# Performance work log

Measured on AMD Instinct MI355X. Metric: run time of the kernel, lower is better.

The kernel has to match this reference:

```python
import jax, jax.numpy as jnp
import numpy as np

DIM, B, H, W = 96, 2, 64, 64
D_INNER, D_STATE, DT_RANK, K = 2 * DIM, 16, 6, 4


def _conv2d(x, w, b=None, padding=0, dilation=1, groups=1):
    out = jax.lax.conv_general_dilated(
        x, w, (1, 1), [(padding, padding)] * 2,
        rhs_dilation=(dilation, dilation),
        dimension_numbers=('NCHW', 'OIHW', 'NCHW'),
        feature_group_count=groups)
    return out if b is None else out + b[None, :, None, None]


def _layernorm(x, g, b, eps=1e-5):
    mu = x.mean(-1, keepdims=True)
    xc = x - mu
    var = (xc * xc).mean(-1, keepdims=True)
    return xc * jax.lax.rsqrt(var + eps) * g + b


def _chan_recal(t, w1, w2):
    s = t.mean((2, 3)) + t.max(axis=(2, 3))          # GAP + GMP, (B,C)
    w = jax.nn.sigmoid(jax.nn.relu(s @ w1.T) @ w2.T)
    return t * w[:, :, None, None]


def _selective_scan(u, delta, A, Bm, Cm, D):
    # u, delta: (B,K,d,L); A: (K,d,N); Bm,Cm: (B,K,N,L); D: (K,d)
    Bsz, Kk, d, L = u.shape
    N = A.shape[-1]
    seq = (jnp.moveaxis(delta, -1, 0), jnp.moveaxis(u, -1, 0),
           jnp.moveaxis(Bm, -1, 0), jnp.moveaxis(Cm, -1, 0))
    h0 = jnp.zeros((Bsz, Kk, d, N), u.dtype)

    def step(h, inp):
        dl, ul, bl, cl = inp  # (B,K,d),(B,K,d),(B,K,N),(B,K,N)
        h = jnp.exp(dl[..., None] * A) * h + (dl * ul)[..., None] * bl[:, :, None, :]
        return h, (h * cl[:, :, None, :]).sum(-1)

    _, ys = jax.lax.scan(step, h0, seq)
    return jnp.moveaxis(ys, 0, -1) + D[None, :, :, None] * u  # (B,K,d,L)


def _ss2d(x, in_proj_w, conv_w, conv_b, x_proj_w, dt_w, dt_b,
          A_logs, Ds, out_norm_g, out_norm_b, out_proj_w):
    Bsz, Hh, Ww, C = x.shape
    d = in_proj_w.shape[0] // 2
    xm, z = jnp.split(x @ in_proj_w.T, 2, axis=-1)
    xm = jnp.transpose(xm, (0, 3, 1, 2))  # (B,d,H,W)
    xm = jax.nn.silu(_conv2d(xm, conv_w, conv_b, padding=1, groups=d))
    L = Hh * Ww
    x_hw = xm.reshape(Bsz, d, L)
    x_wh = jnp.transpose(xm, (0, 1, 3, 2)).reshape(Bsz, d, L)
    xs = jnp.stack([x_hw, x_wh, x_hw[..., ::-1], x_wh[..., ::-1]], axis=1)  # (B,4,d,L)
    x_dbl = jnp.einsum('bkdl,kcd->bkcl', xs, x_proj_w)
    r = dt_w.shape[-1]
    N = A_logs.shape[-1]
    dts, Bs, Cs = jnp.split(x_dbl, [r, r + N], axis=2)
    dts = jax.nn.softplus(jnp.einsum('bkrl,kdr->bkdl', dts, dt_w) + dt_b[None, :, :, None])
    out_y = _selective_scan(xs, dts, -jnp.exp(A_logs), Bs, Cs, Ds)
    inv_y = out_y[:, 2:4, :, ::-1]
    wh = lambda t: jnp.transpose(t.reshape(Bsz, d, Ww, Hh), (0, 1, 3, 2)).reshape(Bsz, d, L)
    y = out_y[:, 0] + inv_y[:, 0] + wh(out_y[:, 1]) + wh(inv_y[:, 1])
    y = _layernorm(jnp.transpose(y, (0, 2, 1)).reshape(Bsz, Hh, Ww, d), out_norm_g, out_norm_b)
    return (y * jax.nn.silu(z)) @ out_proj_w.T


def _forward(x, arf_w1, arf_b1, arf_w2, arf_b2, arf_w3, arf_b3, arf_w4, arf_b4,
             fuse_w, fuse_b, edge_w, enh_w1, enh_b1, bn_g, bn_b, enh_w2, enh_b2,
             pre_fc1, pre_fc2, norm_g, norm_b, in_proj_w, ss_conv_w, ss_conv_b,
             x_proj_w, dt_w, dt_b, A_logs, Ds, out_norm_g, out_norm_b, out_proj_w,
             post_fc1, post_fc2, proj_w, proj_b):
    shortcut = x
    C = x.shape[1]
    g = C // 4
    # AdaptiveReceptiveField (fc gating branch is dead code in the original forward)
    f1 = _conv2d(x, arf_w1, arf_b1, padding=1, dilation=1, groups=g)
    f2 = _conv2d(x, arf_w2, arf_b2, padding=2, dilation=2, groups=g)
    f3 = _conv2d(x, arf_w3, arf_b3, padding=4, dilation=4, groups=g)
    f4 = _conv2d(x, arf_w4, arf_b4, padding=8, dilation=8, groups=g)
    h = _conv2d(jnp.concatenate([f1, f2, f3, f4], 1), fuse_w, fuse_b)
    # LearnableEdgeEnhancement (BatchNorm in training mode: batch stats, biased var)
    edge = _conv2d(h, edge_w, None, padding=1, groups=C)
    e = _conv2d(edge, enh_w1, enh_b1)
    mu = e.mean((0, 2, 3), keepdims=True)
    var = ((e - mu) ** 2).mean((0, 2, 3), keepdims=True)
    e = jax.nn.relu((e - mu) * jax.lax.rsqrt(var + 1e-5) * bn_g[None, :, None, None]
                    + bn_b[None, :, None, None])
    h = h * (1.0 + jax.nn.sigmoid(_conv2d(e, enh_w2, enh_b2)))
    h = _chan_recal(h, pre_fc1, pre_fc2)
    hn = _layernorm(jnp.transpose(h, (0, 2, 3, 1)), norm_g, norm_b)
    hn = _ss2d(hn, in_proj_w, ss_conv_w, ss_conv_b, x_proj_w, dt_w, dt_b,
               A_logs, Ds, out_norm_g, out_norm_b, out_proj_w)
    h = jnp.transpose(hn, (0, 3, 1, 2))
    h = _chan_recal(h, post_fc1, post_fc2)
    h = _conv2d(h, proj_w, proj_b)
    return shortcut + h


def setup_inputs():
    key = jax.random.key(0)
    ks = iter(jax.random.split(key, 48))
    rn = lambda shape, s=0.05: jax.random.normal(next(ks), shape, jnp.float32) * s
    lap = jnp.array([[0., 1., 0.], [1., -4., 1.], [0., 1., 0.]], jnp.float32)
    q = DIM // 4
    inp = {
        'x': jax.random.normal(next(ks), (B, DIM, H, W), jnp.float32),
        'arf_w1': rn((q, 4, 3, 3)), 'arf_b1': rn((q,)),
        'arf_w2': rn((q, 4, 3, 3)), 'arf_b2': rn((q,)),
        'arf_w3': rn((q, 4, 3, 3)), 'arf_b3': rn((q,)),
        'arf_w4': rn((q, 4, 3, 3)), 'arf_b4': rn((q,)),
        'fuse_w': rn((DIM, DIM, 1, 1)), 'fuse_b': rn((DIM,)),
        'edge_w': jnp.tile(lap[None, None], (DIM, 1, 1, 1)),
        'enh_w1': rn((q, DIM, 1, 1)), 'enh_b1': rn((q,)),
        'bn_g': jnp.ones((q,), jnp.float32), 'bn_b': jnp.zeros((q,), jnp.float32),
        'enh_w2': rn((DIM, q, 1, 1)), 'enh_b2': rn((DIM,)),
        'pre_fc1': rn((q, DIM)), 'pre_fc2': rn((DIM, q)),
        'norm_g': jnp.ones((DIM,), jnp.float32), 'norm_b': jnp.zeros((DIM,), jnp.float32),
        'in_proj_w': rn((2 * D_INNER, DIM)),
        'ss_conv_w': rn((D_INNER, 1, 3, 3)), 'ss_conv_b': rn((D_INNER,)),
        'x_proj_w': rn((K, DT_RANK + 2 * D_STATE, D_INNER)),
        'dt_w': rn((K, D_INNER, DT_RANK), 0.1), 'dt_b': rn((K, D_INNER), 0.1),
        'A_logs': jnp.broadcast_to(jnp.log(jnp.arange(1, D_STATE + 1, dtype=jnp.float32)),
                                   (K, D_INNER, D_STATE)) + jnp.zeros((K, D_INNER, D_STATE), jnp.float32),
        'Ds': jnp.ones((K, D_INNER), jnp.float32),
        'out_norm_g': jnp.ones((D_INNER,), jnp.float32),
        'out_norm_b': jnp.zeros((D_INNER,), jnp.float32),
        'out_proj_w': rn((DIM, D_INNER)),
        'post_fc1': rn((q, DIM)), 'post_fc2': rn((DIM, q)),
        'proj_w': rn((DIM, DIM, 1, 1)), 'proj_b': rn((DIM,)),
    }
    return inp


def reference(x, arf_w1, arf_b1, arf_w2, arf_b2, arf_w3, arf_b3, arf_w4, arf_b4,
              fuse_w, fuse_b, edge_w, enh_w1, enh_b1, bn_g, bn_b, enh_w2, enh_b2,
              pre_fc1, pre_fc2, norm_g, norm_b, in_proj_w, ss_conv_w, ss_conv_b,
              x_proj_w, dt_w, dt_b, A_logs, Ds, out_norm_g, out_norm_b, out_proj_w,
              post_fc1, post_fc2, proj_w, proj_b):
    return _forward(x, arf_w1, arf_b1, arf_w2, arf_b2, arf_w3, arf_b3, arf_w4, arf_b4,
                    fuse_w, fuse_b, edge_w, enh_w1, enh_b1, bn_g, bn_b, enh_w2, enh_b2,
                    pre_fc1, pre_fc2, norm_g, norm_b, in_proj_w, ss_conv_w, ss_conv_b,
                    x_proj_w, dt_w, dt_b, A_logs, Ds, out_norm_g, out_norm_b, out_proj_w,
                    post_fc1, post_fc2, proj_w, proj_b)
```

## Files before the change

kernel.cpp:

```cpp
#include <hip/hip_runtime.h>
#include <cmath>

#define LL   4096
#define HWD  64
#define CCH  96
#define QQ   24
#define DDI  192
#define NST  16
#define NCH  128
#define CLEN 32
#define TSC  32
#define XT2  32
#define XP   108
#define FP   100

static const size_t OFF_F   = 0;
static const size_t OFF_H   = 786432;
static const size_t OFF_E   = 1572864;
static const size_t OFF_BN  = 1769472;
static const size_t OFF_S1  = 1769536;
static const size_t OFF_W1  = 1769728;
static const size_t OFF_S2  = 1769920;
static const size_t OFF_W2  = 1770112;
static const size_t OFF_HN  = 1770304;
static const size_t OFF_XM  = 2556736;
static const size_t OFF_Z   = 4129600;
static const size_t OFF_XC  = 5702464;
static const size_t OFF_DTS = 7275328;
static const size_t OFF_BC  = 13566784;
static const size_t OFF_YK  = 14615360;
static const size_t OFF_Y2  = 22528832;
static const size_t OFF_HL  = 23315264;
static const size_t OFF_SD  = 26460992;
static const size_t OFF_HIN = 26657600;

static __device__ __forceinline__ int map_k(int k, int l) {
  int ll = (k & 2) ? (LL - 1 - l) : l;
  return (k & 1) ? (((ll & 63) << 6) | (ll >> 6)) : ll;
}

__global__ __launch_bounds__(256) void k_arf(const float* __restrict__ x,
    const float* __restrict__ w1, const float* __restrict__ b1,
    const float* __restrict__ w2, const float* __restrict__ b2,
    const float* __restrict__ w3, const float* __restrict__ b3,
    const float* __restrict__ w4, const float* __restrict__ b4,
    float* __restrict__ f) {
  int idx = blockIdx.x * 256 + threadIdx.x;
  int p = idx & (LL - 1);
  int oc = __builtin_amdgcn_readfirstlane((idx >> 12) % CCH);
  int b  = __builtin_amdgcn_readfirstlane(idx / (CCH * LL));
  int i = oc / QQ, q = oc % QQ;
  int dil = 1 << i;
  const float* w  = (i == 0 ? w1 : i == 1 ? w2 : i == 2 ? w3 : w4) + q * 36;
  const float* bb = (i == 0 ? b1 : i == 1 ? b2 : i == 2 ? b3 : b4);
  int yy0 = p >> 6, xx0 = p & 63;
  float acc = bb[q];
  const float* xin = x + ((size_t)b * CCH + q * 4) * LL;
  #pragma unroll
  for (int ky = 0; ky < 3; ky++) {
    int yy = yy0 + (ky - 1) * dil;
    if (yy < 0 || yy >= HWD) continue;
    #pragma unroll
    for (int kx = 0; kx < 3; kx++) {
      int xx = xx0 + (kx - 1) * dil;
      if (xx < 0 || xx >= HWD) continue;
      int pp = (yy << 6) + xx;
      #pragma unroll
      for (int ci = 0; ci < 4; ci++)
        acc += w[ci * 9 + ky * 3 + kx] * xin[(size_t)ci * LL + pp];
    }
  }
  f[idx] = acc;
}

__global__ __launch_bounds__(256) void k_fuse(const float* __restrict__ f,
    const float* __restrict__ fw, const float* __restrict__ fb, float* __restrict__ h) {
  int pix0 = blockIdx.x * 64;
  int oc0 = blockIdx.y * 48;
  int b = pix0 >> 12, p0 = pix0 & (LL - 1);
  int t = threadIdx.x;
  __shared__ float fs[64][FP];
  __shared__ float wbuf[48 * 96];
  for (int i = t; i < 96 * 16; i += 256) {
    int c = i >> 4, q = i & 15;
    float4 v = *(const float4*)(f + ((size_t)b * CCH + c) * LL + p0 + q * 4);
    fs[q * 4 + 0][c] = v.x; fs[q * 4 + 1][c] = v.y;
    fs[q * 4 + 2][c] = v.z; fs[q * 4 + 3][c] = v.w;
  }
  {
    const float4* src = (const float4*)(fw + (size_t)oc0 * CCH);
    float4* dst = (float4*)wbuf;
    for (int i = t; i < 48 * 24; i += 256) dst[i] = src[i];
  }
  __syncthreads();
  int px = t & 63;
  int cg = __builtin_amdgcn_readfirstlane(t >> 6);
  float acc[12];
  #pragma unroll
  for (int j = 0; j < 12; j++) acc[j] = 0.f;
  for (int c4 = 0; c4 < 24; c4++) {
    float4 xv = *(const float4*)(&fs[px][c4 * 4]);
    #pragma unroll
    for (int j = 0; j < 12; j++) {
      float4 wv = *(const float4*)(&wbuf[(cg * 12 + j) * 96 + c4 * 4]);
      acc[j] = fmaf(xv.x, wv.x, fmaf(xv.y, wv.y, fmaf(xv.z, wv.z, fmaf(xv.w, wv.w, acc[j]))));
    }
  }
  __syncthreads();
  float* ot = &fs[0][0];
  #pragma unroll
  for (int j = 0; j < 12; j++) ot[px * 49 + cg * 12 + j] = acc[j];
  __syncthreads();
  for (int i = t; i < 48 * 64; i += 256) {
    int o = i >> 6, p2 = i & 63;
    h[((size_t)b * CCH + oc0 + o) * LL + p0 + p2] = ot[p2 * 49 + o] + fb[oc0 + o];
  }
}

__global__ __launch_bounds__(256) void k_edge(const float* __restrict__ h,
    const float* __restrict__ ew, float* __restrict__ edge) {
  int idx = blockIdx.x * 256 + threadIdx.x;
  int p = idx & (LL - 1);
  int c = __builtin_amdgcn_readfirstlane((idx >> 12) % CCH);
  int b = __builtin_amdgcn_readfirstlane(idx / (CCH * LL));
  int yy0 = p >> 6, xx0 = p & 63;
  const float* w = ew + c * 9;
  const float* hr = h + ((size_t)b * CCH + c) * LL;
  float acc = 0.f;
  #pragma unroll
  for (int ky = 0; ky < 3; ky++) {
    int yy = yy0 + ky - 1;
    if (yy < 0 || yy >= HWD) continue;
    #pragma unroll
    for (int kx = 0; kx < 3; kx++) {
      int xx = xx0 + kx - 1;
      if (xx < 0 || xx >= HWD) continue;
      acc += w[ky * 3 + kx] * hr[(yy << 6) + xx];
    }
  }
  edge[idx] = acc;
}

__global__ __launch_bounds__(256) void k_e1(const float* __restrict__ edge,
    const float* __restrict__ w, const float* __restrict__ bias, float* __restrict__ e) {
  int idx = blockIdx.x * 256 + threadIdx.x;
  int p = idx & (LL - 1);
  int q = __builtin_amdgcn_readfirstlane((idx >> 12) % QQ);
  int b = __builtin_amdgcn_readfirstlane(idx / (QQ * LL));
  const float* er = edge + (size_t)b * CCH * LL + p;
  const float* wr = w + q * CCH;
  float acc = bias[q];
  for (int c = 0; c < CCH; c++) acc += wr[c] * er[(size_t)c * LL];
  e[idx] = acc;
}

__global__ __launch_bounds__(256) void k_bnstats(const float* __restrict__ e,
    const float* __restrict__ g, const float* __restrict__ bb, float* __restrict__ bn) {
  int q = blockIdx.x, tid = threadIdx.x;
  __shared__ float rs[256], r2[256];
  float s = 0.f, s2 = 0.f;
  for (int b = 0; b < 2; b++) {
    const float* er = e + ((size_t)b * QQ + q) * LL;
    for (int p = tid; p < LL; p += 256) { float v = er[p]; s += v; s2 += v * v; }
  }
  rs[tid] = s; r2[tid] = s2; __syncthreads();
  for (int st = 128; st > 0; st >>= 1) {
    if (tid < st) { rs[tid] += rs[tid + st]; r2[tid] += r2[tid + st]; }
    __syncthreads();
  }
  if (tid == 0) {
    float mu = rs[0] / (2.f * LL);
    float var = r2[0] / (2.f * LL) - mu * mu;
    float sc = g[q] * rsqrtf(var + 1e-5f);
    bn[q] = sc;
    bn[QQ + q] = bb[q] - mu * sc;
  }
}

__global__ __launch_bounds__(256) void k_enh(const float* __restrict__ e,
    const float* __restrict__ bn, const float* __restrict__ w2,
    const float* __restrict__ b2, float* __restrict__ h) {
  int idx = blockIdx.x * 256 + threadIdx.x;
  int p = idx & (LL - 1);
  int o = __builtin_amdgcn_readfirstlane((idx >> 12) % CCH);
  int b = __builtin_amdgcn_readfirstlane(idx / (CCH * LL));
  const float* er = e + (size_t)b * QQ * LL + p;
  const float* wr = w2 + o * QQ;
  float acc = b2[o];
  #pragma unroll
  for (int q = 0; q < QQ; q++) {
    float en = fmaxf(er[(size_t)q * LL] * bn[q] + bn[QQ + q], 0.f);
    acc += wr[q] * en;
  }
  float sig = 1.f / (1.f + __expf(-acc));
  h[idx] *= (1.f + sig);
}

__global__ __launch_bounds__(256) void k_rowreduce(const float* __restrict__ t, float* __restrict__ sout) {
  int row = blockIdx.x, tid = threadIdx.x;
  __shared__ float rs[256], rm[256];
  float s = 0.f, m = -3.402823466e38f;
  const float* tr = t + (size_t)row * LL;
  for (int p = tid; p < LL; p += 256) { float v = tr[p]; s += v; m = fmaxf(m, v); }
  rs[tid] = s; rm[tid] = m; __syncthreads();
  for (int st = 128; st > 0; st >>= 1) {
    if (tid < st) { rs[tid] += rs[tid + st]; rm[tid] = fmaxf(rm[tid], rm[tid + st]); }
    __syncthreads();
  }
  if (tid == 0) sout[row] = rs[0] / (float)LL + rm[0];
}

__global__ __launch_bounds__(128) void k_recal_fc(const float* __restrict__ s1,
    const float* __restrict__ fc1, const float* __restrict__ fc2, float* __restrict__ wout) {
  int b = blockIdx.x, tid = threadIdx.x;
  __shared__ float sv[CCH];
  __shared__ float hid[QQ];
  if (tid < CCH) sv[tid] = s1[b * CCH + tid];
  __syncthreads();
  if (tid < QQ) {
    float a = 0.f;
    for (int c = 0; c < CCH; c++) a += sv[c] * fc1[tid * CCH + c];
    hid[tid] = fmaxf(a, 0.f);
  }
  __syncthreads();
  if (tid < CCH) {
    float a = 0.f;
    #pragma unroll
    for (int q = 0; q < QQ; q++) a += hid[q] * fc2[tid * QQ + q];
    wout[b * CCH + tid] = 1.f / (1.f + __expf(-a));
  }
}

__global__ __launch_bounds__(256) void k_recal_ln(const float* __restrict__ h,
    const float* __restrict__ w1buf, const float* __restrict__ ng,
    const float* __restrict__ nb, float* __restrict__ hn) {
  int pix = blockIdx.x * 4 + (threadIdx.x >> 6);
  int b = pix >> 12, p = pix & (LL - 1);
  int l = threadIdx.x & 63;
  float v0 = h[((size_t)b * CCH + l) * LL + p] * w1buf[b * CCH + l];
  float v1 = 0.f;
  if (l < 32) v1 = h[((size_t)b * CCH + 64 + l) * LL + p] * w1buf[b * CCH + 64 + l];
  float s = v0 + v1;
  #pragma unroll
  for (int o = 32; o > 0; o >>= 1) s += __shfl_xor(s, o);
  float mu = s / (float)CCH;
  float q = (v0 - mu) * (v0 - mu);
  if (l < 32) q += (v1 - mu) * (v1 - mu);
  #pragma unroll
  for (int o = 32; o > 0; o >>= 1) q += __shfl_xor(q, o);
  float rs = rsqrtf(q / (float)CCH + 1e-5f);
  float* dst = hn + ((size_t)b * LL + p) * CCH;
  dst[l] = (v0 - mu) * rs * ng[l] + nb[l];
  if (l < 32) dst[64 + l] = (v1 - mu) * rs * ng[64 + l] + nb[64 + l];
}

__global__ __launch_bounds__(256) void k_inproj(const float* __restrict__ hn,
    const float* __restrict__ W, float* __restrict__ xm, float* __restrict__ z) {
  int pix0 = blockIdx.x * 64;
  int oc0 = blockIdx.y * CCH;
  int t = threadIdx.x;
  __shared__ float xs[64][XP];
  __shared__ float wbuf[CCH * CCH];
  for (int i = t; i < 64 * 24; i += 256) {
    int row = i / 24, dq = i % 24;
    *(float4*)(&xs[row][dq * 4]) = *(const float4*)(hn + (size_t)(pix0 + row) * CCH + dq * 4);
  }
  {
    const float4* src = (const float4*)(W + (size_t)oc0 * CCH);
    float4* dst = (float4*)wbuf;
    for (int i = t; i < CCH * 24; i += 256) dst[i] = src[i];
  }
  __syncthreads();
  int li = t & 63;
  int cg = __builtin_amdgcn_readfirstlane(t >> 6);
  float acc[24];
  #pragma unroll
  for (int j = 0; j < 24; j++) acc[j] = 0.f;
  for (int dq = 0; dq < 24; dq++) {
    float4 xv = *(const float4*)(&xs[li][dq * 4]);
    #pragma unroll
    for (int j = 0; j < 24; j++) {
      float4 wv = *(const float4*)(&wbuf[(cg + 4 * j) * CCH + dq * 4]);
      acc[j] = fmaf(xv.x, wv.x, fmaf(xv.y, wv.y, fmaf(xv.z, wv.z, fmaf(xv.w, wv.w, acc[j]))));
    }
  }
  __syncthreads();
  float* ot = &xs[0][0];
  #pragma unroll
  for (int j = 0; j < 24; j++) ot[li * 97 + cg + 4 * j] = acc[j];
  __syncthreads();
  float* dst = (oc0 < DDI) ? xm : z;
  int od0 = oc0 % DDI;
  for (int i = t; i < 64 * 96; i += 256) {
    int row = i / 96, c = i % 96;
    dst[(size_t)(pix0 + row) * DDI + od0 + c] = ot[row * 97 + c];
  }
}

__global__ __launch_bounds__(256) void k_ssconv(const float* __restrict__ xm,
    const float* __restrict__ w, const float* __restrict__ bias, float* __restrict__ xc) {
  int idx = blockIdx.x * 256 + threadIdx.x;
  int d = idx % DDI;
  int rem = idx / DDI;
  int xx0 = rem & 63;
  int y0 = ((rem >> 6) & 31) * 2;
  int b = idx / (DDI * LL / 2);
  float wv[9];
  #pragma unroll
  for (int i = 0; i < 9; i++) wv[i] = w[d * 9 + i];
  float acc0 = bias[d], acc1 = bias[d];
  const float* xr = xm + (size_t)b * LL * DDI + d;
  #pragma unroll
  for (int ky = -1; ky <= 2; ky++) {
    int yy = y0 + ky;
    if (yy < 0 || yy >= HWD) continue;
    #pragma unroll
    for (int kx = -1; kx <= 1; kx++) {
      int xx = xx0 + kx;
      if (xx < 0 || xx >= HWD) continue;
      float val = xr[(size_t)((yy << 6) + xx) * DDI];
      if (ky <= 1) acc0 += wv[(ky + 1) * 3 + (kx + 1)] * val;
      if (ky >= 0) acc1 += wv[ky * 3 + (kx + 1)] * val;
    }
  }
  size_t o0 = ((size_t)b * LL + (y0 << 6) + xx0) * DDI + d;
  xc[o0] = acc0 / (1.f + __expf(-acc0));
  xc[o0 + 64 * DDI] = acc1 / (1.f + __expf(-acc1));
}

__global__ __launch_bounds__(256) void k_xdbl(const float* __restrict__ xc,
    const float* __restrict__ xpw, float* __restrict__ dtr_ws, float* __restrict__ bcb) {
  int lt = blockIdx.x;
  int bk = blockIdx.y;
  int b = bk >> 2, k = bk & 3;
  int t = threadIdx.x;
  __shared__ float xs[XT2][XP];
  __shared__ float wbuf[38 * 96];
  int l0 = lt * XT2;
  int pos = t & 31;
  int cg = t >> 5;
  float acc[5];
  #pragma unroll
  for (int j = 0; j < 5; j++) acc[j] = 0.f;
  for (int h = 0; h < 2; h++) {
    __syncthreads();
    for (int i = t; i < XT2 * 24; i += 256) {
      int row = i / 24, dq = i % 24;
      int p = map_k(k, l0 + row);
      *(float4*)(&xs[row][dq * 4]) =
          *(const float4*)(xc + ((size_t)b * LL + p) * DDI + h * 96 + dq * 4);
    }
    for (int i = t; i < 38 * 24; i += 256) {
      int c = i / 24, dq = i % 24;
      *(float4*)(&wbuf[c * 96 + dq * 4]) =
          *(const float4*)(xpw + ((size_t)k * 38 + c) * DDI + h * 96 + dq * 4);
    }
    __syncthreads();
    for (int dq = 0; dq < 24; dq++) {
      float4 xv = *(const float4*)(&xs[pos][dq * 4]);
      #pragma unroll
      for (int j = 0; j < 5; j++) {
        int c = cg + 8 * j;
        if (c < 38) {
          float4 wv = *(const float4*)(&wbuf[c * 96 + dq * 4]);
          acc[j] = fmaf(xv.x, wv.x, fmaf(xv.y, wv.y, fmaf(xv.z, wv.z, fmaf(xv.w, wv.w, acc[j]))));
        }
      }
    }
  }
  #pragma unroll
  for (int j = 0; j < 5; j++) {
    int c = cg + 8 * j;
    if (c < 6) dtr_ws[((size_t)bk * LL + l0 + pos) * 6 + c] = acc[j];
    else if (c < 38) bcb[((size_t)bk * LL + l0 + pos) * 32 + (c - 6)] = acc[j];
  }
}

template <int PASS>
__global__ __launch_bounds__(192) void k_scan(const float* __restrict__ dtr_ws,
    const float* __restrict__ bcb, const float* __restrict__ xc,
    const float* __restrict__ A_logs, const float* __restrict__ dtw,
    const float* __restrict__ dtb, float* __restrict__ hl, float* __restrict__ sd,
    const float* __restrict__ hin, float* __restrict__ yk) {
  int ch = blockIdx.x, bk = blockIdx.y;
  int b = bk >> 2, k = bk & 3;
  int d = threadIdx.x;
  __shared__ float u_s[TSC][DDI];
  __shared__ float bcs[TSC][32];
  __shared__ float dtr_s[TSC][6];
  float Av[NST];
  #pragma unroll
  for (int n = 0; n < NST; n++) Av[n] = -__expf(A_logs[(size_t)(k * DDI + d) * NST + n]);
  bool pw = true;
  #pragma unroll
  for (int n = 1; n < NST; n++) pw = pw && (fabsf(Av[n] - (float)(n + 1) * Av[0]) <= 1e-3f * (n + 1));
  float wdt[6];
  #pragma unroll
  for (int r = 0; r < 6; r++) wdt[r] = dtw[((size_t)(k * DDI + d)) * 6 + r];
  float bdt = dtb[k * DDI + d];
  float h[NST];
  if (PASS == 0) {
    #pragma unroll
    for (int n = 0; n < NST; n++) h[n] = 0.f;
  } else {
    const float* hp = hin + ((size_t)(bk * DDI + d) * NCH + ch) * NST;
    #pragma unroll
    for (int n = 0; n < NST; n++) h[n] = hp[n];
  }
  float sumdt = 0.f;
  int l0 = ch * CLEN;
  {
    for (int i = d; i < TSC * (DDI / 4); i += 192) {
      int row = i / (DDI / 4), q = i % (DDI / 4);
      int p = map_k(k, l0 + row);
      ((float4*)u_s)[i] = *(const float4*)(xc + ((size_t)b * LL + p) * DDI + q * 4);
    }
    {
      const float4* src = (const float4*)(bcb + ((size_t)bk * LL + l0) * 32);
      float4* dst = (float4*)bcs;
      for (int i = d; i < TSC * 32 / 4; i += 192) dst[i] = src[i];
    }
    for (int i = d; i < TSC * 6; i += 192)
      ((float*)dtr_s)[i] = dtr_ws[((size_t)bk * LL + l0) * 6 + i];
    __syncthreads();
    for (int tt = 0; tt < TSC; tt++) {
      float a = bdt;
      #pragma unroll
      for (int r = 0; r < 6; r++) a = fmaf(wdt[r], dtr_s[tt][r], a);
      float dt = (a > 15.f) ? a : __logf(1.f + __expf(a));
      float u  = u_s[tt][d];
      float dtu = dt * u;
      if (PASS == 0) sumdt += dt;
      float eA[NST];
      if (pw) {
        float E = __expf(dt * Av[0]);
        float en = 1.f;
        #pragma unroll
        for (int n = 0; n < NST; n++) { en *= E; eA[n] = en; }
      } else {
        #pragma unroll
        for (int n = 0; n < NST; n++) eA[n] = __expf(dt * Av[n]);
      }
      float y = 0.f;
      #pragma unroll
      for (int n = 0; n < NST; n++) {
        h[n] = eA[n] * h[n] + dtu * bcs[tt][n];
        y += h[n] * bcs[tt][16 + n];
      }
      if (PASS == 1) {
        int p = map_k(k, l0 + tt);
        yk[((size_t)bk * LL + p) * DDI + d] = y;
      }
    }
  }
  if (PASS == 0) {
    float* hp = hl + ((size_t)(bk * DDI + d) * NCH + ch) * NST;
    #pragma unroll
    for (int n = 0; n < NST; n++) hp[n] = h[n];
    sd[(size_t)(bk * DDI + d) * NCH + ch] = sumdt;
  }
}

__global__ __launch_bounds__(256) void k_carry(const float* __restrict__ A_logs,
    const float* __restrict__ hl, const float* __restrict__ sd, float* __restrict__ hin) {
  int idx = blockIdx.x * 256 + threadIdx.x;
  int n = idx & 15;
  int d = (idx >> 4) % DDI;
  int bk = idx / (DDI * NST);
  int k = bk & 3;
  float Aval = -__expf(A_logs[(size_t)(k * DDI + d) * NST + n]);
  float h = 0.f;
  size_t base = (size_t)(bk * DDI + d) * NCH;
  for (int ch = 0; ch < NCH; ch++) {
    hin[(base + ch) * NST + n] = h;
    h = __expf(Aval * sd[base + ch]) * h + hl[(base + ch) * NST + n];
  }
}

__global__ __launch_bounds__(256) void k_combine(const float* __restrict__ yk,
    const float* __restrict__ xc, const float* __restrict__ Ds, const float* __restrict__ z,
    const float* __restrict__ ong, const float* __restrict__ onb, float* __restrict__ g) {
  int pix = blockIdx.x * 4 + (threadIdx.x >> 6);
  int b = pix >> 12, p = pix & (LL - 1);
  int l = threadIdx.x & 63;
  float v[3];
  #pragma unroll
  for (int m = 0; m < 3; m++) {
    int d = l + 64 * m;
    size_t base = ((size_t)b * 4 * LL + p) * DDI + d;
    float tv = yk[base] + yk[base + (size_t)LL * DDI] + yk[base + 2ul * LL * DDI] + yk[base + 3ul * LL * DDI];
    tv += (Ds[d] + Ds[DDI + d] + Ds[2 * DDI + d] + Ds[3 * DDI + d]) * xc[((size_t)b * LL + p) * DDI + d];
    v[m] = tv;
  }
  float s = v[0] + v[1] + v[2];
  #pragma unroll
  for (int o = 32; o > 0; o >>= 1) s += __shfl_xor(s, o);
  float mu = s / (float)DDI;
  float q = 0.f;
  #pragma unroll
  for (int m = 0; m < 3; m++) q += (v[m] - mu) * (v[m] - mu);
  #pragma unroll
  for (int o = 32; o > 0; o >>= 1) q += __shfl_xor(q, o);
  float rs = rsqrtf(q / (float)DDI + 1e-5f);
  #pragma unroll
  for (int m = 0; m < 3; m++) {
    int d = l + 64 * m;
    float yv = (v[m] - mu) * rs * ong[d] + onb[d];
    float zz = z[((size_t)b * LL + p) * DDI + d];
    g[((size_t)b * LL + p) * DDI + d] = yv * (zz / (1.f + __expf(-zz)));
  }
}

__global__ __launch_bounds__(256) void k_outproj(const float* __restrict__ g,
    const float* __restrict__ W, float* __restrict__ y2) {
  int pix0 = blockIdx.x * 64;
  int oc0 = blockIdx.y * 48;
  int b = pix0 >> 12, p0 = pix0 & (LL - 1);
  int t = threadIdx.x;
  __shared__ float xs[64][XP];
  __shared__ float wbuf[48 * 96];
  int li = t & 63;
  int cg = __builtin_amdgcn_readfirstlane(t >> 6);
  float acc[12];
  #pragma unroll
  for (int j = 0; j < 12; j++) acc[j] = 0.f;
  for (int h = 0; h < 2; h++) {
    __syncthreads();
    for (int i = t; i < 64 * 24; i += 256) {
      int row = i / 24, dq = i % 24;
      *(float4*)(&xs[row][dq * 4]) =
          *(const float4*)(g + (size_t)(pix0 + row) * DDI + h * 96 + dq * 4);
    }
    for (int i = t; i < 48 * 24; i += 256) {
      int c = i / 24, dq = i % 24;
      *(float4*)(&wbuf[c * 96 + dq * 4]) =
          *(const float4*)(W + (size_t)(oc0 + c) * DDI + h * 96 + dq * 4);
    }
    __syncthreads();
    for (int dq = 0; dq < 24; dq++) {
      float4 xv = *(const float4*)(&xs[li][dq * 4]);
      #pragma unroll
      for (int j = 0; j < 12; j++) {
        float4 wv = *(const float4*)(&wbuf[(cg + 4 * j) * 96 + dq * 4]);
        acc[j] = fmaf(xv.x, wv.x, fmaf(xv.y, wv.y, fmaf(xv.z, wv.z, fmaf(xv.w, wv.w, acc[j]))));
      }
    }
  }
  __syncthreads();
  float* ot = &xs[0][0];
  #pragma unroll
  for (int j = 0; j < 12; j++) ot[li * 49 + cg + 4 * j] = acc[j];
  __syncthreads();
  for (int i = t; i < 48 * 64; i += 256) {
    int o = i / 64, pi = i % 64;
    y2[((size_t)b * CCH + oc0 + o) * LL + p0 + pi] = ot[pi * 49 + o];
  }
}

__global__ __launch_bounds__(256) void k_final(const float* __restrict__ x,
    const float* __restrict__ y2, const float* __restrict__ w2buf,
    const float* __restrict__ pw, const float* __restrict__ pb, float* __restrict__ out) {
  int pix0 = blockIdx.x * 64;
  int oc0 = blockIdx.y * 48;
  int b = pix0 >> 12, p0 = pix0 & (LL - 1);
  int t = threadIdx.x;
  __shared__ float fs[64][FP];
  __shared__ float wbuf[48 * 96];
  for (int i = t; i < 96 * 16; i += 256) {
    int c = i >> 4, q = i & 15;
    float4 v = *(const float4*)(y2 + ((size_t)b * CCH + c) * LL + p0 + q * 4);
    fs[q * 4 + 0][c] = v.x; fs[q * 4 + 1][c] = v.y;
    fs[q * 4 + 2][c] = v.z; fs[q * 4 + 3][c] = v.w;
  }
  for (int i = t; i < 48 * 24; i += 256) {
    int row = i / 24, q = i % 24;
    float4 wv = *(const float4*)(pw + (size_t)(oc0 + row) * CCH + q * 4);
    float4 cv = *(const float4*)(w2buf + b * CCH + q * 4);
    ((float4*)wbuf)[i] = make_float4(wv.x * cv.x, wv.y * cv.y, wv.z * cv.z, wv.w * cv.w);
  }
  __syncthreads();
  int px = t & 63;
  int cg = __builtin_amdgcn_readfirstlane(t >> 6);
  float acc[12];
  #pragma unroll
  for (int j = 0; j < 12; j++) acc[j] = 0.f;
  for (int c4 = 0; c4 < 24; c4++) {
    float4 xv = *(const float4*)(&fs[px][c4 * 4]);
    #pragma unroll
    for (int j = 0; j < 12; j++) {
      float4 wv = *(const float4*)(&wbuf[(cg * 12 + j) * 96 + c4 * 4]);
      acc[j] = fmaf(xv.x, wv.x, fmaf(xv.y, wv.y, fmaf(xv.z, wv.z, fmaf(xv.w, wv.w, acc[j]))));
    }
  }
  __syncthreads();
  float* ot = &fs[0][0];
  #pragma unroll
  for (int j = 0; j < 12; j++) ot[px * 49 + cg * 12 + j] = acc[j];
  __syncthreads();
  for (int i = t; i < 48 * 64; i += 256) {
    int o = i >> 6, p2 = i & 63;
    size_t oi = ((size_t)b * CCH + oc0 + o) * LL + p0 + p2;
    out[oi] = x[oi] + pb[oc0 + o] + ot[p2 * 49 + o];
  }
}

extern "C" void kernel_launch(void* const* d_in, const int* in_sizes, int n_in,
                              void* d_out, int out_size, void* d_ws, size_t ws_size,
                              hipStream_t stream) {
  const float* x        = (const float*)d_in[0];
  const float* arf_w1   = (const float*)d_in[1];
  const float* arf_b1   = (const float*)d_in[2];
  const float* arf_w2   = (const float*)d_in[3];
  const float* arf_b2   = (const float*)d_in[4];
  const float* arf_w3   = (const float*)d_in[5];
  const float* arf_b3   = (const float*)d_in[6];
  const float* arf_w4   = (const float*)d_in[7];
  const float* arf_b4   = (const float*)d_in[8];
  const float* fuse_w   = (const float*)d_in[9];
  const float* fuse_b   = (const float*)d_in[10];
  const float* edge_w   = (const float*)d_in[11];
  const float* enh_w1   = (const float*)d_in[12];
  const float* enh_b1   = (const float*)d_in[13];
  const float* bn_g     = (const float*)d_in[14];
  const float* bn_b     = (const float*)d_in[15];
  const float* enh_w2   = (const float*)d_in[16];
  const float* enh_b2   = (const float*)d_in[17];
  const float* pre_fc1  = (const float*)d_in[18];
  const float* pre_fc2  = (const float*)d_in[19];
  const float* norm_g   = (const float*)d_in[20];
  const float* norm_b   = (const float*)d_in[21];
  const float* in_proj_w= (const float*)d_in[22];
  const float* ss_conv_w= (const float*)d_in[23];
  const float* ss_conv_b= (const float*)d_in[24];
  const float* x_proj_w = (const float*)d_in[25];
  const float* dt_w     = (const float*)d_in[26];
  const float* dt_b     = (const float*)d_in[27];
  const float* A_logs   = (const float*)d_in[28];
  const float* Ds       = (const float*)d_in[29];
  const float* out_ng   = (const float*)d_in[30];
  const float* out_nb   = (const float*)d_in[31];
  const float* out_proj_w = (const float*)d_in[32];
  const float* post_fc1 = (const float*)d_in[33];
  const float* post_fc2 = (const float*)d_in[34];
  const float* proj_w   = (const float*)d_in[35];
  const float* proj_b   = (const float*)d_in[36];

  float* ws = (float*)d_ws;
  float* fbuf  = ws + OFF_F;
  float* hbuf  = ws + OFF_H;
  float* ebuf  = ws + OFF_E;
  float* bnbuf = ws + OFF_BN;
  float* s1buf = ws + OFF_S1;
  float* w1buf = ws + OFF_W1;
  float* s2buf = ws + OFF_S2;
  float* w2buf = ws + OFF_W2;
  float* hnbuf = ws + OFF_HN;
  float* xmbuf = ws + OFF_XM;
  float* zbuf  = ws + OFF_Z;
  float* xcbuf = ws + OFF_XC;
  float* dtrbuf= ws + OFF_DTS;
  float* bcbuf = ws + OFF_BC;
  float* ykbuf = ws + OFF_YK;
  float* hlbuf = ws + OFF_HL;
  float* sdbuf = ws + OFF_SD;
  float* hinbuf= ws + OFF_HIN;
  float* y2buf = ws + OFF_Y2;
  float* gbuf  = xmbuf;

  k_arf<<<3072, 256, 0, stream>>>(x, arf_w1, arf_b1, arf_w2, arf_b2, arf_w3, arf_b3, arf_w4, arf_b4, fbuf);
  k_fuse<<<dim3(128, 2), 256, 0, stream>>>(fbuf, fuse_w, fuse_b, hbuf);
  k_edge<<<3072, 256, 0, stream>>>(hbuf, edge_w, fbuf);
  k_e1<<<768, 256, 0, stream>>>(fbuf, enh_w1, enh_b1, ebuf);
  k_bnstats<<<24, 256, 0, stream>>>(ebuf, bn_g, bn_b, bnbuf);
  k_enh<<<3072, 256, 0, stream>>>(ebuf, bnbuf, enh_w2, enh_b2, hbuf);
  k_rowreduce<<<192, 256, 0, stream>>>(hbuf, s1buf);
  k_recal_fc<<<2, 128, 0, stream>>>(s1buf, pre_fc1, pre_fc2, w1buf);
  k_recal_ln<<<2048, 256, 0, stream>>>(hbuf, w1buf, norm_g, norm_b, hnbuf);
  k_inproj<<<dim3(128, 4), 256, 0, stream>>>(hnbuf, in_proj_w, xmbuf, zbuf);
  k_ssconv<<<3072, 256, 0, stream>>>(xmbuf, ss_conv_w, ss_conv_b, xcbuf);
  k_xdbl<<<dim3(LL / XT2, 8), 256, 0, stream>>>(xcbuf, x_proj_w, dtrbuf, bcbuf);
  k_scan<0><<<dim3(NCH, 8), 192, 0, stream>>>(dtrbuf, bcbuf, xcbuf, A_logs, dt_w, dt_b, hlbuf, sdbuf, nullptr, nullptr);
  k_carry<<<96, 256, 0, stream>>>(A_logs, hlbuf, sdbuf, hinbuf);
  k_scan<1><<<dim3(NCH, 8), 192, 0, stream>>>(dtrbuf, bcbuf, xcbuf, A_logs, dt_w, dt_b, nullptr, nullptr, hinbuf, ykbuf);
  k_combine<<<2048, 256, 0, stream>>>(ykbuf, xcbuf, Ds, zbuf, out_ng, out_nb, gbuf);
  k_outproj<<<dim3(128, 2), 256, 0, stream>>>(gbuf, out_proj_w, y2buf);
  k_rowreduce<<<192, 256, 0, stream>>>(y2buf, s2buf);
  k_recal_fc<<<2, 128, 0, stream>>>(s2buf, post_fc1, post_fc2, w2buf);
  k_final<<<dim3(128, 2), 256, 0, stream>>>(x, y2buf, w2buf, proj_w, proj_b, (float*)d_out);
  (void)in_sizes; (void)n_in; (void)out_size; (void)ws_size;
}
```

Baseline: 241.7 us.

## Fuse channel-recalibration reductions, FC and layernorms into neighbouring GEMM kernels

Global sum/max reductions now come from per-block partials written by k_enh and k_outproj. The recalibration FC layers are recomputed inside each consuming block of k_inproj and k_final. The pre-norm layernorm moves into k_inproj, and the combine plus out_norm plus SiLU gating moves into k_outproj. This removes six launches and the intermediate hn and g round trips through global memory. In exchange, every block redundantly runs the small FC layers, the variance is computed in a single pass, and the shared-memory footprint grows.

```diff
diff --git a/kernel.cpp b/kernel.cpp
--- a/kernel.cpp
+++ b/kernel.cpp
@@ -13,16 +13,12 @@
 #define XT2  32
 #define XP   108
 #define FP   100
+#define VP   204
 
 static const size_t OFF_F   = 0;
 static const size_t OFF_H   = 786432;
 static const size_t OFF_E   = 1572864;
 static const size_t OFF_BN  = 1769472;
-static const size_t OFF_S1  = 1769536;
-static const size_t OFF_W1  = 1769728;
-static const size_t OFF_S2  = 1769920;
-static const size_t OFF_W2  = 1770112;
-static const size_t OFF_HN  = 1770304;
 static const size_t OFF_XM  = 2556736;
 static const size_t OFF_Z   = 4129600;
 static const size_t OFF_XC  = 5702464;
@@ -33,6 +29,10 @@
 static const size_t OFF_HL  = 23315264;
 static const size_t OFF_SD  = 26460992;
 static const size_t OFF_HIN = 26657600;
+static const size_t OFF_S1PS= 29803328;
+static const size_t OFF_S1PM= 29806400;
+static const size_t OFF_S2PS= 29809472;
+static const size_t OFF_S2PM= 29821760;
 
 static __device__ __forceinline__ int map_k(int k, int l) {
   int ll = (k & 2) ? (LL - 1 - l) : l;
@@ -179,8 +179,10 @@
 
 __global__ __launch_bounds__(256) void k_enh(const float* __restrict__ e,
     const float* __restrict__ bn, const float* __restrict__ w2,
-    const float* __restrict__ b2, float* __restrict__ h) {
-  int idx = blockIdx.x * 256 + threadIdx.x;
+    const float* __restrict__ b2, float* __restrict__ h,
+    float* __restrict__ s1ps, float* __restrict__ s1pm) {
+  int tid = threadIdx.x;
+  int idx = blockIdx.x * 256 + tid;
   int p = idx & (LL - 1);
   int o = __builtin_amdgcn_readfirstlane((idx >> 12) % CCH);
   int b = __builtin_amdgcn_readfirstlane(idx / (CCH * LL));
@@ -193,82 +195,96 @@
     acc += wr[q] * en;
   }
   float sig = 1.f / (1.f + __expf(-acc));
-  h[idx] *= (1.f + sig);
-}
-
-__global__ __launch_bounds__(256) void k_rowreduce(const float* __restrict__ t, float* __restrict__ sout) {
-  int row = blockIdx.x, tid = threadIdx.x;
-  __shared__ float rs[256], rm[256];
-  float s = 0.f, m = -3.402823466e38f;
-  const float* tr = t + (size_t)row * LL;
-  for (int p = tid; p < LL; p += 256) { float v = tr[p]; s += v; m = fmaxf(m, v); }
-  rs[tid] = s; rm[tid] = m; __syncthreads();
+  float val = h[idx] * (1.f + sig);
+  h[idx] = val;
+  __shared__ float rsum[256], rmax[256];
+  rsum[tid] = val; rmax[tid] = val; __syncthreads();
   for (int st = 128; st > 0; st >>= 1) {
-    if (tid < st) { rs[tid] += rs[tid + st]; rm[tid] = fmaxf(rm[tid], rm[tid + st]); }
+    if (tid < st) { rsum[tid] += rsum[tid + st]; rmax[tid] = fmaxf(rmax[tid], rmax[tid + st]); }
     __syncthreads();
   }
-  if (tid == 0) sout[row] = rs[0] / (float)LL + rm[0];
-}
-
-__global__ __launch_bounds__(128) void k_recal_fc(const float* __restrict__ s1,
-    const float* __restrict__ fc1, const float* __restrict__ fc2, float* __restrict__ wout) {
-  int b = blockIdx.x, tid = threadIdx.x;
-  __shared__ float sv[CCH];
-  __shared__ float hid[QQ];
-  if (tid < CCH) sv[tid] = s1[b * CCH + tid];
-  __syncthreads();
-  if (tid < QQ) {
-    float a = 0.f;
-    for (int c = 0; c < CCH; c++) a += sv[c] * fc1[tid * CCH + c];
-    hid[tid] = fmaxf(a, 0.f);
-  }
-  __syncthreads();
-  if (tid < CCH) {
-    float a = 0.f;
-    #pragma unroll
-    for (int q = 0; q < QQ; q++) a += hid[q] * fc2[tid * QQ + q];
-    wout[b * CCH + tid] = 1.f / (1.f + __expf(-a));
-  }
-}
-
-__global__ __launch_bounds__(256) void k_recal_ln(const float* __restrict__ h,
-    const float* __restrict__ w1buf, const float* __restrict__ ng,
-    const float* __restrict__ nb, float* __restrict__ hn) {
-  int pix = blockIdx.x * 4 + (threadIdx.x >> 6);
-  int b = pix >> 12, p = pix & (LL - 1);
-  int l = threadIdx.x & 63;
-  float v0 = h[((size_t)b * CCH + l) * LL + p] * w1buf[b * CCH + l];
-  float v1 = 0.f;
-  if (l < 32) v1 = h[((size_t)b * CCH + 64 + l) * LL + p] * w1buf[b * CCH + 64 + l];
-  float s = v0 + v1;
-  #pragma unroll
-  for (int o = 32; o > 0; o >>= 1) s += __shfl_xor(s, o);
-  float mu = s / (float)CCH;
-  float q = (v0 - mu) * (v0 - mu);
-  if (l < 32) q += (v1 - mu) * (v1 - mu);
-  #pragma unroll
-  for (int o = 32; o > 0; o >>= 1) q += __shfl_xor(q, o);
-  float rs = rsqrtf(q / (float)CCH + 1e-5f);
-  float* dst = hn + ((size_t)b * LL + p) * CCH;
-  dst[l] = (v0 - mu) * rs * ng[l] + nb[l];
-  if (l < 32) dst[64 + l] = (v1 - mu) * rs * ng[64 + l] + nb[64 + l];
-}
-
-__global__ __launch_bounds__(256) void k_inproj(const float* __restrict__ hn,
+  if (tid == 0) {
+    int row = blockIdx.x >> 4, blk = blockIdx.x & 15;
+    s1ps[row * 16 + blk] = rsum[0];
+    s1pm[row * 16 + blk] = rmax[0];
+  }
+}
+
+__global__ __launch_bounds__(256) void k_inproj(const float* __restrict__ h,
+    const float* __restrict__ s1ps, const float* __restrict__ s1pm,
+    const float* __restrict__ fc1, const float* __restrict__ fc2,
+    const float* __restrict__ ng, const float* __restrict__ nb,
     const float* __restrict__ W, float* __restrict__ xm, float* __restrict__ z) {
   int pix0 = blockIdx.x * 64;
   int oc0 = blockIdx.y * CCH;
+  int b = pix0 >> 12, p0 = pix0 & (LL - 1);
   int t = threadIdx.x;
   __shared__ float xs[64][XP];
   __shared__ float wbuf[CCH * CCH];
-  for (int i = t; i < 64 * 24; i += 256) {
-    int row = i / 24, dq = i % 24;
-    *(float4*)(&xs[row][dq * 4]) = *(const float4*)(hn + (size_t)(pix0 + row) * CCH + dq * 4);
-  }
+  __shared__ float wsm[CCH];
+  __shared__ float hid[QQ];
+  __shared__ float ps[64][4], ps2[64][4];
+  __shared__ float mu_s[64], rs_s[64];
+  if (t < CCH) {
+    const float4* sp = (const float4*)(s1ps + (size_t)(b * CCH + t) * 16);
+    const float4* mp = (const float4*)(s1pm + (size_t)(b * CCH + t) * 16);
+    float s = 0.f, m = -3.402823466e38f;
+    #pragma unroll
+    for (int i = 0; i < 4; i++) {
+      float4 a = sp[i]; s += a.x + a.y + a.z + a.w;
+      float4 c = mp[i]; m = fmaxf(m, fmaxf(fmaxf(c.x, c.y), fmaxf(c.z, c.w)));
+    }
+    wsm[t] = s / (float)LL + m;
+  }
+  __syncthreads();
+  if (t < QQ) {
+    float a = 0.f;
+    for (int c = 0; c < CCH; c++) a += wsm[c] * fc1[t * CCH + c];
+    hid[t] = fmaxf(a, 0.f);
+  }
+  __syncthreads();
+  float w1v = 0.f;
+  if (t < CCH) {
+    float a = 0.f;
+    #pragma unroll
+    for (int q = 0; q < QQ; q++) a += hid[q] * fc2[t * QQ + q];
+    w1v = 1.f / (1.f + __expf(-a));
+  }
+  __syncthreads();
+  if (t < CCH) wsm[t] = w1v;
   {
     const float4* src = (const float4*)(W + (size_t)oc0 * CCH);
     float4* dst = (float4*)wbuf;
     for (int i = t; i < CCH * 24; i += 256) dst[i] = src[i];
+  }
+  __syncthreads();
+  for (int i = t; i < CCH * 16; i += 256) {
+    int c = i >> 4, q = i & 15;
+    float w = wsm[c];
+    float4 v = *(const float4*)(h + ((size_t)b * CCH + c) * LL + p0 + q * 4);
+    xs[q * 4 + 0][c] = v.x * w; xs[q * 4 + 1][c] = v.y * w;
+    xs[q * 4 + 2][c] = v.z * w; xs[q * 4 + 3][c] = v.w * w;
+  }
+  __syncthreads();
+  {
+    int px = t & 63, qr = t >> 6;
+    float s = 0.f, s2 = 0.f;
+    #pragma unroll
+    for (int j = 0; j < 24; j++) { float v = xs[px][qr * 24 + j]; s += v; s2 += v * v; }
+    ps[px][qr] = s; ps2[px][qr] = s2;
+  }
+  __syncthreads();
+  if (t < 64) {
+    float ss = ps[t][0] + ps[t][1] + ps[t][2] + ps[t][3];
+    float ss2 = ps2[t][0] + ps2[t][1] + ps2[t][2] + ps2[t][3];
+    float mu = ss / (float)CCH;
+    mu_s[t] = mu;
+    rs_s[t] = rsqrtf(ss2 / (float)CCH - mu * mu + 1e-5f);
+  }
+  __syncthreads();
+  for (int i = t; i < 64 * CCH; i += 256) {
+    int px = i / CCH, c = i % CCH;
+    xs[px][c] = (xs[px][c] - mu_s[px]) * rs_s[px] * ng[c] + nb[c];
   }
   __syncthreads();
   int li = t & 63;
@@ -477,68 +493,96 @@
   }
 }
 
-__global__ __launch_bounds__(256) void k_combine(const float* __restrict__ yk,
+__global__ __launch_bounds__(256) void k_outproj(const float* __restrict__ yk,
     const float* __restrict__ xc, const float* __restrict__ Ds, const float* __restrict__ z,
-    const float* __restrict__ ong, const float* __restrict__ onb, float* __restrict__ g) {
-  int pix = blockIdx.x * 4 + (threadIdx.x >> 6);
-  int b = pix >> 12, p = pix & (LL - 1);
-  int l = threadIdx.x & 63;
-  float v[3];
-  #pragma unroll
-  for (int m = 0; m < 3; m++) {
-    int d = l + 64 * m;
-    size_t base = ((size_t)b * 4 * LL + p) * DDI + d;
-    float tv = yk[base] + yk[base + (size_t)LL * DDI] + yk[base + 2ul * LL * DDI] + yk[base + 3ul * LL * DDI];
-    tv += (Ds[d] + Ds[DDI + d] + Ds[2 * DDI + d] + Ds[3 * DDI + d]) * xc[((size_t)b * LL + p) * DDI + d];
-    v[m] = tv;
-  }
-  float s = v[0] + v[1] + v[2];
-  #pragma unroll
-  for (int o = 32; o > 0; o >>= 1) s += __shfl_xor(s, o);
-  float mu = s / (float)DDI;
-  float q = 0.f;
-  #pragma unroll
-  for (int m = 0; m < 3; m++) q += (v[m] - mu) * (v[m] - mu);
-  #pragma unroll
-  for (int o = 32; o > 0; o >>= 1) q += __shfl_xor(q, o);
-  float rs = rsqrtf(q / (float)DDI + 1e-5f);
-  #pragma unroll
-  for (int m = 0; m < 3; m++) {
-    int d = l + 64 * m;
-    float yv = (v[m] - mu) * rs * ong[d] + onb[d];
-    float zz = z[((size_t)b * LL + p) * DDI + d];
-    g[((size_t)b * LL + p) * DDI + d] = yv * (zz / (1.f + __expf(-zz)));
-  }
-}
-
-__global__ __launch_bounds__(256) void k_outproj(const float* __restrict__ g,
-    const float* __restrict__ W, float* __restrict__ y2) {
+    const float* __restrict__ ong, const float* __restrict__ onb,
+    const float* __restrict__ W, float* __restrict__ y2,
+    float* __restrict__ s2ps, float* __restrict__ s2pm) {
   int pix0 = blockIdx.x * 64;
   int oc0 = blockIdx.y * 48;
   int b = pix0 >> 12, p0 = pix0 & (LL - 1);
   int t = threadIdx.x;
-  __shared__ float xs[64][XP];
+  __shared__ float xs[64][VP];
   __shared__ float wbuf[48 * 96];
-  int li = t & 63;
-  int cg = __builtin_amdgcn_readfirstlane(t >> 6);
+  __shared__ float dsum[DDI];
+  __shared__ float ps[64][4], ps2[64][4];
+  __shared__ float mu_s[64], rs_s[64];
+  if (t < 48) {
+    float4 a  = *(const float4*)(Ds + t * 4);
+    float4 c1 = *(const float4*)(Ds + DDI + t * 4);
+    float4 c2 = *(const float4*)(Ds + 2 * DDI + t * 4);
+    float4 c3 = *(const float4*)(Ds + 3 * DDI + t * 4);
+    *(float4*)(&dsum[t * 4]) = make_float4(a.x + c1.x + c2.x + c3.x, a.y + c1.y + c2.y + c3.y,
+                                           a.z + c1.z + c2.z + c3.z, a.w + c1.w + c2.w + c3.w);
+  }
+  __syncthreads();
+  int px = t & 63, qr = t >> 6;
+  int p = p0 + px;
+  size_t pb = ((size_t)b * LL + p) * DDI;
+  size_t yb = ((size_t)b * 4 * LL + p) * DDI;
+  {
+    float s = 0.f, s2 = 0.f;
+    #pragma unroll
+    for (int j = 0; j < 12; j++) {
+      int c = (qr * 12 + j) * 4;
+      float4 y0 = *(const float4*)(yk + yb + c);
+      float4 y1 = *(const float4*)(yk + yb + (size_t)LL * DDI + c);
+      float4 y2v = *(const float4*)(yk + yb + 2ul * LL * DDI + c);
+      float4 y3 = *(const float4*)(yk + yb + 3ul * LL * DDI + c);
+      float4 u = *(const float4*)(xc + pb + c);
+      float4 dv = *(const float4*)(&dsum[c]);
+      float4 v;
+      v.x = y0.x + y1.x + y2v.x + y3.x + dv.x * u.x;
+      v.y = y0.y + y1.y + y2v.y + y3.y + dv.y * u.y;
+      v.z = y0.z + y1.z + y2v.z + y3.z + dv.z * u.z;
+      v.w = y0.w + y1.w + y2v.w + y3.w + dv.w * u.w;
+      *(float4*)(&xs[px][c]) = v;
+      s += v.x + v.y + v.z + v.w;
+      s2 += v.x * v.x + v.y * v.y + v.z * v.z + v.w * v.w;
+    }
+    ps[px][qr] = s; ps2[px][qr] = s2;
+  }
+  __syncthreads();
+  if (t < 64) {
+    float ss = ps[t][0] + ps[t][1] + ps[t][2] + ps[t][3];
+    float ss2 = ps2[t][0] + ps2[t][1] + ps2[t][2] + ps2[t][3];
+    float mu = ss / (float)DDI;
+    mu_s[t] = mu;
+    rs_s[t] = rsqrtf(ss2 / (float)DDI - mu * mu + 1e-5f);
+  }
+  __syncthreads();
+  {
+    float mu = mu_s[px], rs = rs_s[px];
+    #pragma unroll
+    for (int j = 0; j < 12; j++) {
+      int c = (qr * 12 + j) * 4;
+      float4 v = *(const float4*)(&xs[px][c]);
+      float4 zz = *(const float4*)(z + pb + c);
+      float4 og = *(const float4*)(ong + c);
+      float4 ob = *(const float4*)(onb + c);
+      float4 gv;
+      gv.x = ((v.x - mu) * rs * og.x + ob.x) * (zz.x / (1.f + __expf(-zz.x)));
+      gv.y = ((v.y - mu) * rs * og.y + ob.y) * (zz.y / (1.f + __expf(-zz.y)));
+      gv.z = ((v.z - mu) * rs * og.z + ob.z) * (zz.z / (1.f + __expf(-zz.z)));
+      gv.w = ((v.w - mu) * rs * og.w + ob.w) * (zz.w / (1.f + __expf(-zz.w)));
+      *(float4*)(&xs[px][c]) = gv;
+    }
+  }
+  int li = px;
+  int cg = __builtin_amdgcn_readfirstlane(qr);
   float acc[12];
   #pragma unroll
   for (int j = 0; j < 12; j++) acc[j] = 0.f;
-  for (int h = 0; h < 2; h++) {
+  for (int hh = 0; hh < 2; hh++) {
     __syncthreads();
-    for (int i = t; i < 64 * 24; i += 256) {
-      int row = i / 24, dq = i % 24;
-      *(float4*)(&xs[row][dq * 4]) =
-          *(const float4*)(g + (size_t)(pix0 + row) * DDI + h * 96 + dq * 4);
-    }
     for (int i = t; i < 48 * 24; i += 256) {
       int c = i / 24, dq = i % 24;
       *(float4*)(&wbuf[c * 96 + dq * 4]) =
-          *(const float4*)(W + (size_t)(oc0 + c) * DDI + h * 96 + dq * 4);
+          *(const float4*)(W + (size_t)(oc0 + c) * DDI + hh * 96 + dq * 4);
     }
     __syncthreads();
     for (int dq = 0; dq < 24; dq++) {
-      float4 xv = *(const float4*)(&xs[li][dq * 4]);
+      float4 xv = *(const float4*)(&xs[li][hh * 96 + dq * 4]);
       #pragma unroll
       for (int j = 0; j < 12; j++) {
         float4 wv = *(const float4*)(&wbuf[(cg + 4 * j) * 96 + dq * 4]);
@@ -546,6 +590,22 @@
       }
     }
   }
+  int lane = t & 63;
+  #pragma unroll
+  for (int j = 0; j < 12; j++) {
+    float sv = acc[j], mv = acc[j];
+    #pragma unroll
+    for (int o = 32; o > 0; o >>= 1) {
+      sv += __shfl_xor(sv, o);
+      mv = fmaxf(mv, __shfl_xor(mv, o));
+    }
+    if (lane == 0) {
+      int oc = oc0 + cg + 4 * j;
+      int tile = blockIdx.x & 63;
+      s2ps[(size_t)(b * CCH + oc) * 64 + tile] = sv;
+      s2pm[(size_t)(b * CCH + oc) * 64 + tile] = mv;
+    }
+  }
   __syncthreads();
   float* ot = &xs[0][0];
   #pragma unroll
@@ -558,7 +618,8 @@
 }
 
 __global__ __launch_bounds__(256) void k_final(const float* __restrict__ x,
-    const float* __restrict__ y2, const float* __restrict__ w2buf,
+    const float* __restrict__ y2, const float* __restrict__ s2ps, const float* __restrict__ s2pm,
+    const float* __restrict__ fc1, const float* __restrict__ fc2,
     const float* __restrict__ pw, const float* __restrict__ pb, float* __restrict__ out) {
   int pix0 = blockIdx.x * 64;
   int oc0 = blockIdx.y * 48;
@@ -566,6 +627,36 @@
   int t = threadIdx.x;
   __shared__ float fs[64][FP];
   __shared__ float wbuf[48 * 96];
+  __shared__ float wsm[CCH];
+  __shared__ float hid[QQ];
+  if (t < CCH) {
+    const float4* sp = (const float4*)(s2ps + (size_t)(b * CCH + t) * 64);
+    const float4* mp = (const float4*)(s2pm + (size_t)(b * CCH + t) * 64);
+    float s = 0.f, m = -3.402823466e38f;
+    #pragma unroll
+    for (int i = 0; i < 16; i++) {
+      float4 a = sp[i]; s += a.x + a.y + a.z + a.w;
+      float4 c = mp[i]; m = fmaxf(m, fmaxf(fmaxf(c.x, c.y), fmaxf(c.z, c.w)));
+    }
+    wsm[t] = s / (float)LL + m;
+  }
+  __syncthreads();
+  if (t < QQ) {
+    float a = 0.f;
+    for (int c = 0; c < CCH; c++) a += wsm[c] * fc1[t * CCH + c];
+    hid[t] = fmaxf(a, 0.f);
+  }
+  __syncthreads();
+  float w2v = 0.f;
+  if (t < CCH) {
+    float a = 0.f;
+    #pragma unroll
+    for (int q = 0; q < QQ; q++) a += hid[q] * fc2[t * QQ + q];
+    w2v = 1.f / (1.f + __expf(-a));
+  }
+  __syncthreads();
+  if (t < CCH) wsm[t] = w2v;
+  __syncthreads();
   for (int i = t; i < 96 * 16; i += 256) {
     int c = i >> 4, q = i & 15;
     float4 v = *(const float4*)(y2 + ((size_t)b * CCH + c) * LL + p0 + q * 4);
@@ -575,8 +666,8 @@
   for (int i = t; i < 48 * 24; i += 256) {
     int row = i / 24, q = i % 24;
     float4 wv = *(const float4*)(pw + (size_t)(oc0 + row) * CCH + q * 4);
-    float4 cv = *(const float4*)(w2buf + b * CCH + q * 4);
-    ((float4*)wbuf)[i] = make_float4(wv.x * cv.x, wv.y * cv.y, wv.z * cv.z, wv.w * cv.w);
+    ((float4*)wbuf)[i] = make_float4(wv.x * wsm[q * 4], wv.y * wsm[q * 4 + 1],
+                                     wv.z * wsm[q * 4 + 2], wv.w * wsm[q * 4 + 3]);
   }
   __syncthreads();
   int px = t & 63;
@@ -650,42 +741,34 @@
   float* hbuf  = ws + OFF_H;
   float* ebuf  = ws + OFF_E;
   float* bnbuf = ws + OFF_BN;
-  float* s1buf = ws + OFF_S1;
-  float* w1buf = ws + OFF_W1;
-  float* s2buf = ws + OFF_S2;
-  float* w2buf = ws + OFF_W2;
-  float* hnbuf = ws + OFF_HN;
   float* xmbuf = ws + OFF_XM;
   float* zbuf  = ws + OFF_Z;
   float* xcbuf = ws + OFF_XC;
   float* dtrbuf= ws + OFF_DTS;
   float* bcbuf = ws + OFF_BC;
   float* ykbuf = ws + OFF_YK;
+  float* y2buf = ws + OFF_Y2;
   float* hlbuf = ws + OFF_HL;
   float* sdbuf = ws + OFF_SD;
   float* hinbuf= ws + OFF_HIN;
-  float* y2buf = ws + OFF_Y2;
-  float* gbuf  = xmbuf;
+  float* s1ps  = ws + OFF_S1PS;
+  float* s1pm  = ws + OFF_S1PM;
+  float* s2ps  = ws + OFF_S2PS;
+  float* s2pm  = ws + OFF_S2PM;
 
   k_arf<<<3072, 256, 0, stream>>>(x, arf_w1, arf_b1, arf_w2, arf_b2, arf_w3, arf_b3, arf_w4, arf_b4, fbuf);
   k_fuse<<<dim3(128, 2), 256, 0, stream>>>(fbuf, fuse_w, fuse_b, hbuf);
   k_edge<<<3072, 256, 0, stream>>>(hbuf, edge_w, fbuf);
   k_e1<<<768, 256, 0, stream>>>(fbuf, enh_w1, enh_b1, ebuf);
   k_bnstats<<<24, 256, 0, stream>>>(ebuf, bn_g, bn_b, bnbuf);
-  k_enh<<<3072, 256, 0, stream>>>(ebuf, bnbuf, enh_w2, enh_b2, hbuf);
-  k_rowreduce<<<192, 256, 0, stream>>>(hbuf, s1buf);
-  k_recal_fc<<<2, 128, 0, stream>>>(s1buf, pre_fc1, pre_fc2, w1buf);
-  k_recal_ln<<<2048, 256, 0, stream>>>(hbuf, w1buf, norm_g, norm_b, hnbuf);
-  k_inproj<<<dim3(128, 4), 256, 0, stream>>>(hnbuf, in_proj_w, xmbuf, zbuf);
+  k_enh<<<3072, 256, 0, stream>>>(ebuf, bnbuf, enh_w2, enh_b2, hbuf, s1ps, s1pm);
+  k_inproj<<<dim3(128, 4), 256, 0, stream>>>(hbuf, s1ps, s1pm, pre_fc1, pre_fc2, norm_g, norm_b, in_proj_w, xmbuf, zbuf);
   k_ssconv<<<3072, 256, 0, stream>>>(xmbuf, ss_conv_w, ss_conv_b, xcbuf);
   k_xdbl<<<dim3(LL / XT2, 8), 256, 0, stream>>>(xcbuf, x_proj_w, dtrbuf, bcbuf);
   k_scan<0><<<dim3(NCH, 8), 192, 0, stream>>>(dtrbuf, bcbuf, xcbuf, A_logs, dt_w, dt_b, hlbuf, sdbuf, nullptr, nullptr);
   k_carry<<<96, 256, 0, stream>>>(A_logs, hlbuf, sdbuf, hinbuf);
   k_scan<1><<<dim3(NCH, 8), 192, 0, stream>>>(dtrbuf, bcbuf, xcbuf, A_logs, dt_w, dt_b, nullptr, nullptr, hinbuf, ykbuf);
-  k_combine<<<2048, 256, 0, stream>>>(ykbuf, xcbuf, Ds, zbuf, out_ng, out_nb, gbuf);
-  k_outproj<<<dim3(128, 2), 256, 0, stream>>>(gbuf, out_proj_w, y2buf);
-  k_rowreduce<<<192, 256, 0, stream>>>(y2buf, s2buf);
-  k_recal_fc<<<2, 128, 0, stream>>>(s2buf, post_fc1, post_fc2, w2buf);
-  k_final<<<dim3(128, 2), 256, 0, stream>>>(x, y2buf, w2buf, proj_w, proj_b, (float*)d_out);
+  k_outproj<<<dim3(128, 2), 256, 0, stream>>>(ykbuf, xcbuf, Ds, zbuf, out_ng, out_nb, out_proj_w, y2buf, s2ps, s2pm);
+  k_final<<<dim3(128, 2), 256, 0, stream>>>(x, y2buf, s2ps, s2pm, post_fc1, post_fc2, proj_w, proj_b, (float*)d_out);
   (void)in_sizes; (void)n_in; (void)out_size; (void)ws_size;
 }
```

New measurement: 228.9 us. 1.06x faster.
